# Optimization experiments

Hardware: AMD Instinct MI355X
Metric: run time of the kernel (lower is better)

Reference implementation:

```python
import jax, jax.numpy as jnp
import numpy as np

H = 16          # nhead
EPS = 1e-5      # LayerNorm eps (torch default)


def _layernorm(x, g, b):
    mu = jnp.mean(x, axis=-1, keepdims=True)
    var = jnp.mean(jnp.square(x - mu), axis=-1, keepdims=True)
    return (x - mu) * jax.lax.rsqrt(var + EPS) * g + b


def setup_inputs() -> dict:
    key = jax.random.key(0)
    ks = jax.random.split(key, 8)
    B, L, D, F = 256, 64, 1024, 4096
    s = 0.02
    return {
        "src": jax.random.normal(ks[0], (B, L, D), jnp.float32),
        "Wq": jax.random.normal(ks[1], (D, D), jnp.float32) * s,
        "bq": jnp.zeros((D,), jnp.float32),
        "Wk": jax.random.normal(ks[2], (D, D), jnp.float32) * s,
        "bk": jnp.zeros((D,), jnp.float32),
        "Wv": jax.random.normal(ks[3], (D, D), jnp.float32) * s,
        "bv": jnp.zeros((D,), jnp.float32),
        "Wo": jax.random.normal(ks[4], (D, D), jnp.float32) * s,
        "bo": jnp.zeros((D,), jnp.float32),
        "rel_bias": jax.random.normal(ks[5], (H, 2 * L - 1), jnp.float32) * s,
        "W1": jax.random.normal(ks[6], (D, F), jnp.float32) * s,
        "b1": jnp.zeros((F,), jnp.float32),
        "W2": jax.random.normal(ks[7], (F, D), jnp.float32) * s,
        "b2": jnp.zeros((D,), jnp.float32),
        "g1": jnp.ones((D,), jnp.float32),
        "be1": jnp.zeros((D,), jnp.float32),
        "g2": jnp.ones((D,), jnp.float32),
        "be2": jnp.zeros((D,), jnp.float32),
    }


def reference(src, Wq, bq, Wk, bk, Wv, bv, Wo, bo, rel_bias,
              W1, b1, W2, b2, g1, be1, g2, be2):
    B, L, D = src.shape
    dh = D // H
    # --- relative multi-head attention ---
    q = (src @ Wq + bq).reshape(B, L, H, dh)
    k = (src @ Wk + bk).reshape(B, L, H, dh)
    v = (src @ Wv + bv).reshape(B, L, H, dh)
    scores = jnp.einsum('bqhd,bkhd->bhqk', q, k) / jnp.sqrt(jnp.float32(dh))
    # relative position bias lookup: index i - j + (L-1) into (H, 2L-1) table
    rel_idx = jnp.arange(L)[:, None] - jnp.arange(L)[None, :] + (L - 1)  # (L,L)
    scores = scores + rel_bias[:, rel_idx]  # broadcast (H,L,L) over batch
    attn = jax.nn.softmax(scores, axis=-1)
    ctx = jnp.einsum('bhqk,bkhd->bqhd', attn, v).reshape(B, L, D)
    attn_out = ctx @ Wo + bo
    # --- residual + LN + FFN + residual + LN (dropout = eval no-op) ---
    x = _layernorm(src + attn_out, g1, be1)
    ff = jax.nn.gelu(x @ W1 + b1) @ W2 + b2
    return _layernorm(x + ff, g2, be2)
```

## Files before the change

### kernel.cpp

```cpp
#include <hip/hip_runtime.h>

typedef __bf16 bf16;
typedef __attribute__((ext_vector_type(8))) __bf16 bf16x8;
typedef __attribute__((ext_vector_type(4))) __bf16 bf16x4;
typedef __attribute__((ext_vector_type(4))) float f32x4;

#define N_TOK 16384
#define DMODEL 1024
#define FDIM 4096
#define NHEAD 16

__device__ __forceinline__ void gload_lds16(const bf16* g, bf16* l) {
  __builtin_amdgcn_global_load_lds(
      (const __attribute__((address_space(1))) void*)g,
      (__attribute__((address_space(3))) void*)l,
      16, 0, 0);
}

__device__ __forceinline__ float gelu_fast(float x) {
  float z2 = 1.5957691216057308f * (x + 0.044715f * x * x * x);
  return x / (1.0f + __expf(-z2));
}

__global__ __launch_bounds__(256) void cvt_copy(const float* __restrict__ x,
                                                bf16* __restrict__ y) {
  size_t i = ((size_t)blockIdx.x * 256 + threadIdx.x) * 8;
  float4 a = *(const float4*)(x + i);
  float4 b = *(const float4*)(x + i + 4);
  bf16x8 o;
  o[0] = (bf16)a.x; o[1] = (bf16)a.y; o[2] = (bf16)a.z; o[3] = (bf16)a.w;
  o[4] = (bf16)b.x; o[5] = (bf16)b.y; o[6] = (bf16)b.z; o[7] = (bf16)b.w;
  *(bf16x8*)(y + i) = o;
}

__global__ void convt(const float* __restrict__ src, bf16* __restrict__ dst,
                      int R, int C) {
  __shared__ float tile[32][33];
  int c0 = blockIdx.x * 32, r0 = blockIdx.y * 32;
  int tx = threadIdx.x, ty = threadIdx.y;
#pragma unroll
  for (int i = 0; i < 4; ++i)
    tile[ty * 4 + i][tx] = src[(size_t)(r0 + ty * 4 + i) * C + c0 + tx];
  __syncthreads();
#pragma unroll
  for (int i = 0; i < 4; ++i)
    dst[(size_t)(c0 + ty * 4 + i) * R + r0 + tx] = (bf16)tile[tx][ty * 4 + i];
}

template <int BM_, int RES, int GELU, int SPLIT3>
__global__ __launch_bounds__(512) void gemm_c(
    const bf16* __restrict__ A, const bf16* __restrict__ BT,
    const float* __restrict__ bias, const float* __restrict__ bias2,
    const float* __restrict__ bias3, const float* __restrict__ resf,
    const bf16* __restrict__ resb, bf16* __restrict__ C,
    bf16* __restrict__ C2, bf16* __restrict__ C3,
    int M, int N, int K) {
  constexpr int ALOADS = BM_ / 64;
  constexpr int MH = BM_ / 32;
  constexpr int MQ = MH / 2;
  __shared__ alignas(16) bf16 sA[2][BM_ * 64];
  __shared__ alignas(16) bf16 sB[2][256 * 64];

  const int tid = threadIdx.x;
  const int lane = tid & 63, wv = tid >> 6;
  const int wr = wv >> 2, wc = wv & 3;
  const int r16 = lane & 15, hk = lane >> 4;

  const int nbn = N >> 8;
  const int cpx = gridDim.x >> 3;
  const int swz = ((int)blockIdx.x & 7) * cpx + ((int)blockIdx.x >> 3);
  const int row0 = (swz / nbn) * BM_, col0 = (swz % nbn) << 8;

  const bf16* Ab = A + (size_t)row0 * K;
  const bf16* Bb = BT + (size_t)col0 * K;

  const bf16* gA[ALOADS];
  const bf16* gB[4];
#pragma unroll
  for (int l = 0; l < ALOADS; ++l) {
    int g = l * 512 + tid, r = g >> 3, p = g & 7;
    gA[l] = Ab + (size_t)r * K + ((p ^ (r & 7)) << 3);
  }
#pragma unroll
  for (int l = 0; l < 4; ++l) {
    int g = l * 512 + tid, r = g >> 3, p = g & 7;
    gB[l] = Bb + (size_t)r * K + ((p ^ (r & 7)) << 3);
  }

  auto stageA = [&](int buf, int kt) {
    const size_t ko = (size_t)kt << 6;
#pragma unroll
    for (int l = 0; l < ALOADS; ++l)
      gload_lds16(gA[l] + ko, &sA[buf][(l * 512 + tid) * 8]);
  };
  auto stageB = [&](int buf, int kt) {
    const size_t ko = (size_t)kt << 6;
#pragma unroll
    for (int l = 0; l < 4; ++l)
      gload_lds16(gB[l] + ko, &sB[buf][(l * 512 + tid) * 8]);
  };
  auto frag = [&](const bf16* s, int row, int kc) -> bf16x8 {
    return *(const bf16x8*)(s + row * 64 + (kc ^ ((row & 7) * 8)));
  };

  f32x4 acc[MH][4] = {};
  bf16x8 aF[MQ][2], bF0[2][2], bF1[2][2];

  const int nt = K >> 6;
  stageA(0, 0); stageB(0, 0);
  stageA(1, 1); stageB(1, 1);
  if constexpr (BM_ == 256) asm volatile("s_waitcnt vmcnt(8)" ::: "memory");
  else                      asm volatile("s_waitcnt vmcnt(6)" ::: "memory");
  __builtin_amdgcn_s_barrier();

  for (int kt = 0; kt < nt; ++kt) {
    const int cb = kt & 1;
    const bf16* sa = &sA[cb][0];
    const bf16* sb = &sB[cb][0];
    const bool pf = (kt + 2 < nt);

#pragma unroll
    for (int m = 0; m < MQ; ++m)
#pragma unroll
      for (int ks = 0; ks < 2; ++ks)
        aF[m][ks] = frag(sa, wr * (BM_ / 2) + m * 16 + r16, ks * 32 + hk * 8);
#pragma unroll
    for (int n = 0; n < 2; ++n)
#pragma unroll
      for (int ks = 0; ks < 2; ++ks)
        bF0[n][ks] = frag(sb, wc * 64 + n * 16 + r16, ks * 32 + hk * 8);
    __builtin_amdgcn_s_barrier();
    __builtin_amdgcn_s_setprio(1);
#pragma unroll
    for (int ks = 0; ks < 2; ++ks)
#pragma unroll
      for (int m = 0; m < MQ; ++m)
#pragma unroll
        for (int n = 0; n < 2; ++n)
          acc[m][n] = __builtin_amdgcn_mfma_f32_16x16x32_bf16(bF0[n][ks], aF[m][ks], acc[m][n], 0, 0, 0);
    __builtin_amdgcn_s_setprio(0);
    __builtin_amdgcn_s_barrier();

#pragma unroll
    for (int n = 0; n < 2; ++n)
#pragma unroll
      for (int ks = 0; ks < 2; ++ks)
        bF1[n][ks] = frag(sb, wc * 64 + (2 + n) * 16 + r16, ks * 32 + hk * 8);
    __builtin_amdgcn_s_barrier();
    __builtin_amdgcn_s_setprio(1);
#pragma unroll
    for (int ks = 0; ks < 2; ++ks)
#pragma unroll
      for (int m = 0; m < MQ; ++m)
#pragma unroll
        for (int n = 0; n < 2; ++n)
          acc[m][2 + n] = __builtin_amdgcn_mfma_f32_16x16x32_bf16(bF1[n][ks], aF[m][ks], acc[m][2 + n], 0, 0, 0);
    __builtin_amdgcn_s_setprio(0);
    __builtin_amdgcn_s_barrier();

#pragma unroll
    for (int m = 0; m < MQ; ++m)
#pragma unroll
      for (int ks = 0; ks < 2; ++ks)
        aF[m][ks] = frag(sa, wr * (BM_ / 2) + (MQ + m) * 16 + r16, ks * 32 + hk * 8);
    if (pf) stageB(cb, kt + 2);
    __builtin_amdgcn_s_barrier();
    __builtin_amdgcn_s_setprio(1);
#pragma unroll
    for (int ks = 0; ks < 2; ++ks)
#pragma unroll
      for (int m = 0; m < MQ; ++m)
#pragma unroll
        for (int n = 0; n < 2; ++n)
          acc[MQ + m][2 + n] = __builtin_amdgcn_mfma_f32_16x16x32_bf16(bF1[n][ks], aF[m][ks], acc[MQ + m][2 + n], 0, 0, 0);
    __builtin_amdgcn_s_setprio(0);
    __builtin_amdgcn_s_barrier();

    if (pf) stageA(cb, kt + 2);
    __builtin_amdgcn_s_setprio(1);
#pragma unroll
    for (int ks = 0; ks < 2; ++ks)
#pragma unroll
      for (int m = 0; m < MQ; ++m)
#pragma unroll
        for (int n = 0; n < 2; ++n)
          acc[MQ + m][n] = __builtin_amdgcn_mfma_f32_16x16x32_bf16(bF0[n][ks], aF[m][ks], acc[MQ + m][n], 0, 0, 0);
    __builtin_amdgcn_s_setprio(0);
    if (pf) {
      if constexpr (BM_ == 256) asm volatile("s_waitcnt vmcnt(8)" ::: "memory");
      else                      asm volatile("s_waitcnt vmcnt(6)" ::: "memory");
    } else if (kt + 1 < nt) {
      asm volatile("s_waitcnt vmcnt(0)" ::: "memory");
    }
    __builtin_amdgcn_s_barrier();
  }

  bf16* Cp = C;
  const float* bp = bias;
  int ldc = N, colb = col0;
  if constexpr (SPLIT3) {
    int grp = col0 >> 10;
    Cp = grp == 0 ? C : (grp == 1 ? C2 : C3);
    bp = grp == 0 ? bias : (grp == 1 ? bias2 : bias3);
    ldc = 1024;
    colb = col0 & 1023;
  }
#pragma unroll
  for (int m = 0; m < MH; ++m) {
    int row = row0 + wr * (BM_ / 2) + m * 16 + r16;
#pragma unroll
    for (int n = 0; n < 4; ++n) {
      int col = colb + wc * 64 + n * 16 + hk * 4;
      f32x4 b4 = *(const f32x4*)&bp[col];
      f32x4 v;
#pragma unroll
      for (int r = 0; r < 4; ++r) v[r] = acc[m][n][r] + b4[r];
      if (RES == 1) {
        f32x4 rr = *(const f32x4*)&resf[(size_t)row * ldc + col];
#pragma unroll
        for (int r = 0; r < 4; ++r) v[r] += rr[r];
      }
      if (RES == 2) {
        bf16x4 rb = *(const bf16x4*)&resb[(size_t)row * ldc + col];
#pragma unroll
        for (int r = 0; r < 4; ++r) v[r] += (float)rb[r];
      }
      bf16x4 o;
#pragma unroll
      for (int r = 0; r < 4; ++r) {
        float x = v[r];
        if (GELU) x = gelu_fast(x);
        o[r] = (bf16)x;
      }
      *(bf16x4*)&Cp[(size_t)row * ldc + col] = o;
    }
  }
}

__global__ __launch_bounds__(256) void attn_k(
    const bf16* q, const bf16* __restrict__ k,
    const bf16* __restrict__ v, const float* __restrict__ rel,
    bf16* ctx) {
  __shared__ alignas(16) bf16 lQ[64 * 64];
  __shared__ alignas(16) bf16 lK[64 * 64];
  __shared__ alignas(16) bf16 lVt[64 * 64];
  __shared__ alignas(16) bf16 lP[4][16 * 64];
  __shared__ float lrel[128];

  const int bh = blockIdx.x;
  const int b = bh >> 4, h = bh & 15;
  const int tid = threadIdx.x;
  const size_t base = (size_t)(b * 64) * DMODEL + h * 64;

#pragma unroll
  for (int i = 0; i < 2; ++i) {
    int j = (tid >> 3) + i * 32;
    int d0 = (tid & 7) * 8;
    *(bf16x8*)&lQ[j * 64 + d0] = *(const bf16x8*)(q + base + (size_t)j * DMODEL + d0);
    *(bf16x8*)&lK[j * 64 + d0] = *(const bf16x8*)(k + base + (size_t)j * DMODEL + d0);
    bf16x8 vvv = *(const bf16x8*)(v + base + (size_t)j * DMODEL + d0);
#pragma unroll
    for (int u = 0; u < 8; ++u) lVt[(d0 + u) * 64 + j] = vvv[u];
  }
  if (tid < 127) lrel[tid] = rel[h * 127 + tid];
  __syncthreads();

  const int lane = tid & 63, w = tid >> 6;
  const int r16 = lane & 15, hk = lane >> 4;

  f32x4 s[4] = {};
#pragma unroll
  for (int dstep = 0; dstep < 2; ++dstep) {
    bf16x8 aq = *(const bf16x8*)&lQ[(w * 16 + r16) * 64 + dstep * 32 + hk * 8];
#pragma unroll
    for (int n = 0; n < 4; ++n) {
      bf16x8 bk_ = *(const bf16x8*)&lK[(n * 16 + r16) * 64 + dstep * 32 + hk * 8];
      s[n] = __builtin_amdgcn_mfma_f32_16x16x32_bf16(aq, bk_, s[n], 0, 0, 0);
    }
  }

  float p[16];
#pragma unroll
  for (int n = 0; n < 4; ++n)
#pragma unroll
    for (int r = 0; r < 4; ++r) {
      int i = w * 16 + hk * 4 + r;
      int j = n * 16 + r16;
      p[n * 4 + r] = s[n][r] * 0.125f + lrel[i - j + 63];
    }
#pragma unroll
  for (int r = 0; r < 4; ++r) {
    float m = fmaxf(fmaxf(p[r], p[4 + r]), fmaxf(p[8 + r], p[12 + r]));
#pragma unroll
    for (int off = 1; off < 16; off <<= 1) m = fmaxf(m, __shfl_xor(m, off));
    float sum = 0.f;
#pragma unroll
    for (int n = 0; n < 4; ++n) {
      p[n * 4 + r] = __expf(p[n * 4 + r] - m);
      sum += p[n * 4 + r];
    }
#pragma unroll
    for (int off = 1; off < 16; off <<= 1) sum += __shfl_xor(sum, off);
    float inv = 1.0f / sum;
#pragma unroll
    for (int n = 0; n < 4; ++n) p[n * 4 + r] *= inv;
  }
#pragma unroll
  for (int n = 0; n < 4; ++n)
#pragma unroll
    for (int r = 0; r < 4; ++r)
      lP[w][(hk * 4 + r) * 64 + n * 16 + r16] = (bf16)p[n * 4 + r];
  __syncthreads();

  f32x4 o[4] = {};
#pragma unroll
  for (int ks = 0; ks < 2; ++ks) {
    bf16x8 ap = *(const bf16x8*)&lP[w][r16 * 64 + ks * 32 + hk * 8];
#pragma unroll
    for (int n = 0; n < 4; ++n) {
      bf16x8 bv_ = *(const bf16x8*)&lVt[(n * 16 + r16) * 64 + ks * 32 + hk * 8];
      o[n] = __builtin_amdgcn_mfma_f32_16x16x32_bf16(ap, bv_, o[n], 0, 0, 0);
    }
  }
#pragma unroll
  for (int n = 0; n < 4; ++n)
#pragma unroll
    for (int r = 0; r < 4; ++r) {
      int trow = b * 64 + w * 16 + hk * 4 + r;
      ctx[(size_t)trow * DMODEL + h * 64 + n * 16 + r16] = (bf16)o[n][r];
    }
}

template <int F32OUT>
__global__ __launch_bounds__(256) void layernorm_k(
    const bf16* __restrict__ x, const float* __restrict__ g,
    const float* __restrict__ be, bf16* __restrict__ ob,
    float* __restrict__ of) {
  int row = blockIdx.x * 4 + (threadIdx.x >> 6);
  int lane = threadIdx.x & 63;
  const bf16* xr = x + (size_t)row * DMODEL + lane * 16;
  bf16x8 v0 = *(const bf16x8*)xr;
  bf16x8 v1 = *(const bf16x8*)(xr + 8);
  float f[16];
#pragma unroll
  for (int j = 0; j < 8; ++j) { f[j] = (float)v0[j]; f[8 + j] = (float)v1[j]; }
  float s = 0.f, sq = 0.f;
#pragma unroll
  for (int j = 0; j < 16; ++j) { s += f[j]; sq += f[j] * f[j]; }
#pragma unroll
  for (int off = 1; off < 64; off <<= 1) {
    s += __shfl_xor(s, off);
    sq += __shfl_xor(sq, off);
  }
  float mean = s * (1.0f / DMODEL);
  float var = sq * (1.0f / DMODEL) - mean * mean;
  float rstd = rsqrtf(var + 1e-5f);
  const float* gp = g + lane * 16;
  const float* bp = be + lane * 16;
  if (F32OUT) {
    float* op = of + (size_t)row * DMODEL + lane * 16;
#pragma unroll
    for (int j = 0; j < 16; ++j)
      op[j] = (f[j] - mean) * rstd * gp[j] + bp[j];
  } else {
    bf16x8 o0, o1;
#pragma unroll
    for (int j = 0; j < 8; ++j) {
      o0[j] = (bf16)((f[j] - mean) * rstd * gp[j] + bp[j]);
      o1[j] = (bf16)((f[8 + j] - mean) * rstd * gp[8 + j] + bp[8 + j]);
    }
    bf16* op = ob + (size_t)row * DMODEL + lane * 16;
    *(bf16x8*)op = o0;
    *(bf16x8*)(op + 8) = o1;
  }
}

extern "C" void kernel_launch(void* const* d_in, const int* in_sizes, int n_in,
                              void* d_out, int out_size, void* d_ws, size_t ws_size,
                              hipStream_t stream) {
  (void)in_sizes; (void)n_in; (void)out_size;
  const float* src = (const float*)d_in[0];
  const float* Wq  = (const float*)d_in[1];
  const float* bq  = (const float*)d_in[2];
  const float* Wk  = (const float*)d_in[3];
  const float* bk  = (const float*)d_in[4];
  const float* Wv  = (const float*)d_in[5];
  const float* bv  = (const float*)d_in[6];
  const float* Wo  = (const float*)d_in[7];
  const float* bo  = (const float*)d_in[8];
  const float* rel = (const float*)d_in[9];
  const float* W1  = (const float*)d_in[10];
  const float* b1  = (const float*)d_in[11];
  const float* W2  = (const float*)d_in[12];
  const float* b2  = (const float*)d_in[13];
  const float* g1  = (const float*)d_in[14];
  const float* be1 = (const float*)d_in[15];
  const float* g2  = (const float*)d_in[16];
  const float* be2 = (const float*)d_in[17];

  char* ws = (char*)d_ws;
  const size_t MiB = 1ull << 20;
  bf16* srcb = (bf16*)(ws + 0 * MiB);
  bf16* qb   = (bf16*)(ws + 32 * MiB);
  bf16* WqT  = (bf16*)(ws + 64 * MiB);
  bf16* WkT  = (bf16*)(ws + 66 * MiB);
  bf16* WvT  = (bf16*)(ws + 68 * MiB);
  bf16* WoT  = (bf16*)(ws + 70 * MiB);
  bf16* W1T  = (bf16*)(ws + 72 * MiB);
  bf16* W2T  = (bf16*)(ws + 80 * MiB);
  bf16* hbuf = (bf16*)(ws + 0 * MiB);
  float* lnout = (float*)(ws + 0 * MiB);
  bf16* kb = (bf16*)d_out;
  bf16* vb = (bf16*)((char*)d_out + 32 * MiB);
  bf16* y1 = kb;
  bf16* xb = vb;
  const bool bigws = (ws_size >= 121 * MiB);
  bf16* y2 = bigws ? (bf16*)(ws + 88 * MiB) : kb;

  cvt_copy<<<(N_TOK * DMODEL) / 2048, 256, 0, stream>>>(src, srcb);
  dim3 tb(32, 8);
  convt<<<dim3(32, 32), tb, 0, stream>>>(Wq, WqT, 1024, 1024);
  convt<<<dim3(32, 32), tb, 0, stream>>>(Wk, WkT, 1024, 1024);
  convt<<<dim3(32, 32), tb, 0, stream>>>(Wv, WvT, 1024, 1024);
  convt<<<dim3(32, 32), tb, 0, stream>>>(Wo, WoT, 1024, 1024);
  convt<<<dim3(128, 32), tb, 0, stream>>>(W1, W1T, 1024, 4096);
  convt<<<dim3(32, 128), tb, 0, stream>>>(W2, W2T, 4096, 1024);

  const int gQKV3 = (N_TOK / 256) * (3072 / 256);
  gemm_c<256, 0, 0, 1><<<gQKV3, 512, 0, stream>>>(
      srcb, WqT, bq, bk, bv, nullptr, nullptr, qb, kb, vb, N_TOK, 3072, DMODEL);

  attn_k<<<256 * NHEAD, 256, 0, stream>>>(qb, kb, vb, rel, qb);

  const int gD = (N_TOK / 256) * (DMODEL / 256);
  gemm_c<256, 1, 0, 0><<<gD, 512, 0, stream>>>(
      qb, WoT, bo, nullptr, nullptr, src, nullptr, y1, nullptr, nullptr, N_TOK, DMODEL, DMODEL);
  layernorm_k<0><<<N_TOK / 4, 256, 0, stream>>>(y1, g1, be1, xb, nullptr);

  const int CH = 8192;
  const int gF1 = (CH / 256) * (FDIM / 256);
  const int gF2 = (CH / 128) * (DMODEL / 256);
  for (int c = 0; c < 2; ++c) {
    const bf16* xc = xb + (size_t)c * CH * DMODEL;
    bf16* yc = y2 + (size_t)c * CH * DMODEL;
    gemm_c<256, 0, 1, 0><<<gF1, 512, 0, stream>>>(
        xc, W1T, b1, nullptr, nullptr, nullptr, nullptr, hbuf, nullptr, nullptr, CH, FDIM, DMODEL);
    gemm_c<128, 2, 0, 0><<<gF2, 512, 0, stream>>>(
        hbuf, W2T, b2, nullptr, nullptr, nullptr, xc, yc, nullptr, nullptr, CH, DMODEL, FDIM);
  }
  if (bigws) {
    layernorm_k<1><<<N_TOK / 4, 256, 0, stream>>>(y2, g2, be2, nullptr, (float*)d_out);
  } else {
    layernorm_k<1><<<N_TOK / 4, 256, 0, stream>>>(y2, g2, be2, nullptr, lnout);
    hipMemcpyAsync(d_out, lnout, (size_t)N_TOK * DMODEL * 4, hipMemcpyDeviceToDevice, stream);
  }
}
```

Measured before the change: 613.3 us.

## Software-pipeline LDS fragment reads across k-tiles in GEMM main loop

Restructures the GEMM k-loop so the low-half A and B fragments for the next k-tile are read from the other LDS buffer while the current tile's last MFMA phases run. The loop is unrolled by two with ping-pong fragment registers, and the global prefetch order is changed to B before A. This aims to hide LDS read latency behind MFMA work. It adds register pressure, a vmcnt(0) wait in every tile, and assumes an even number of k-tiles.

```diff
diff --git a/kernel.cpp b/kernel.cpp
--- a/kernel.cpp
+++ b/kernel.cpp
@@ -56,8 +56,8 @@
     bf16* __restrict__ C2, bf16* __restrict__ C3,
     int M, int N, int K) {
   constexpr int ALOADS = BM_ / 64;
-  constexpr int MH = BM_ / 32;
-  constexpr int MQ = MH / 2;
+  constexpr int MQ = BM_ / 64;
+  constexpr int MH = 2 * MQ;
   __shared__ alignas(16) bf16 sA[2][BM_ * 64];
   __shared__ alignas(16) bf16 sB[2][256 * 64];
 
@@ -104,96 +104,97 @@
   };
 
   f32x4 acc[MH][4] = {};
-  bf16x8 aF[MQ][2], bF0[2][2], bF1[2][2];
+  bf16x8 aL[MQ][2], aH[MQ][2], bH[2][2], bLa[2][2], bLb[2][2];
 
   const int nt = K >> 6;
-  stageA(0, 0); stageB(0, 0);
-  stageA(1, 1); stageB(1, 1);
+  stageB(0, 0); stageA(0, 0);
+  stageB(1, 1); stageA(1, 1);
   if constexpr (BM_ == 256) asm volatile("s_waitcnt vmcnt(8)" ::: "memory");
   else                      asm volatile("s_waitcnt vmcnt(6)" ::: "memory");
   __builtin_amdgcn_s_barrier();
-
-  for (int kt = 0; kt < nt; ++kt) {
-    const int cb = kt & 1;
-    const bf16* sa = &sA[cb][0];
-    const bf16* sb = &sB[cb][0];
-    const bool pf = (kt + 2 < nt);
-
-#pragma unroll
-    for (int m = 0; m < MQ; ++m)
-#pragma unroll
-      for (int ks = 0; ks < 2; ++ks)
-        aF[m][ks] = frag(sa, wr * (BM_ / 2) + m * 16 + r16, ks * 32 + hk * 8);
-#pragma unroll
-    for (int n = 0; n < 2; ++n)
-#pragma unroll
-      for (int ks = 0; ks < 2; ++ks)
-        bF0[n][ks] = frag(sb, wc * 64 + n * 16 + r16, ks * 32 + hk * 8);
-    __builtin_amdgcn_s_barrier();
-    __builtin_amdgcn_s_setprio(1);
+#pragma unroll
+  for (int m = 0; m < MQ; ++m)
 #pragma unroll
     for (int ks = 0; ks < 2; ++ks)
-#pragma unroll
-      for (int m = 0; m < MQ; ++m)
-#pragma unroll
-        for (int n = 0; n < 2; ++n)
-          acc[m][n] = __builtin_amdgcn_mfma_f32_16x16x32_bf16(bF0[n][ks], aF[m][ks], acc[m][n], 0, 0, 0);
-    __builtin_amdgcn_s_setprio(0);
-    __builtin_amdgcn_s_barrier();
-
-#pragma unroll
-    for (int n = 0; n < 2; ++n)
-#pragma unroll
-      for (int ks = 0; ks < 2; ++ks)
-        bF1[n][ks] = frag(sb, wc * 64 + (2 + n) * 16 + r16, ks * 32 + hk * 8);
-    __builtin_amdgcn_s_barrier();
-    __builtin_amdgcn_s_setprio(1);
+      aL[m][ks] = frag(&sA[0][0], wr * (BM_ / 2) + m * 16 + r16, ks * 32 + hk * 8);
+#pragma unroll
+  for (int n = 0; n < 2; ++n)
 #pragma unroll
     for (int ks = 0; ks < 2; ++ks)
-#pragma unroll
-      for (int m = 0; m < MQ; ++m)
-#pragma unroll
-        for (int n = 0; n < 2; ++n)
-          acc[m][2 + n] = __builtin_amdgcn_mfma_f32_16x16x32_bf16(bF1[n][ks], aF[m][ks], acc[m][2 + n], 0, 0, 0);
-    __builtin_amdgcn_s_setprio(0);
-    __builtin_amdgcn_s_barrier();
-
-#pragma unroll
-    for (int m = 0; m < MQ; ++m)
-#pragma unroll
-      for (int ks = 0; ks < 2; ++ks)
-        aF[m][ks] = frag(sa, wr * (BM_ / 2) + (MQ + m) * 16 + r16, ks * 32 + hk * 8);
-    if (pf) stageB(cb, kt + 2);
-    __builtin_amdgcn_s_barrier();
-    __builtin_amdgcn_s_setprio(1);
-#pragma unroll
-    for (int ks = 0; ks < 2; ++ks)
-#pragma unroll
-      for (int m = 0; m < MQ; ++m)
-#pragma unroll
-        for (int n = 0; n < 2; ++n)
-          acc[MQ + m][2 + n] = __builtin_amdgcn_mfma_f32_16x16x32_bf16(bF1[n][ks], aF[m][ks], acc[MQ + m][2 + n], 0, 0, 0);
-    __builtin_amdgcn_s_setprio(0);
-    __builtin_amdgcn_s_barrier();
-
-    if (pf) stageA(cb, kt + 2);
-    __builtin_amdgcn_s_setprio(1);
-#pragma unroll
-    for (int ks = 0; ks < 2; ++ks)
-#pragma unroll
-      for (int m = 0; m < MQ; ++m)
-#pragma unroll
-        for (int n = 0; n < 2; ++n)
-          acc[MQ + m][n] = __builtin_amdgcn_mfma_f32_16x16x32_bf16(bF0[n][ks], aF[m][ks], acc[MQ + m][n], 0, 0, 0);
-    __builtin_amdgcn_s_setprio(0);
-    if (pf) {
-      if constexpr (BM_ == 256) asm volatile("s_waitcnt vmcnt(8)" ::: "memory");
-      else                      asm volatile("s_waitcnt vmcnt(6)" ::: "memory");
-    } else if (kt + 1 < nt) {
-      asm volatile("s_waitcnt vmcnt(0)" ::: "memory");
-    }
-    __builtin_amdgcn_s_barrier();
-  }
+      bLa[n][ks] = frag(&sB[0][0], wc * 64 + n * 16 + r16, ks * 32 + hk * 8);
+
+#define TILE_BODY(t, sa, sb, saN, sbN, bLcur, bLnxt)                           \
+  {                                                                            \
+    const bool rd1 = ((t) + 1 < nt), st2 = ((t) + 2 < nt);                     \
+                                       \
+    _Pragma("unroll") for (int n = 0; n < 2; ++n)                              \
+      _Pragma("unroll") for (int ks = 0; ks < 2; ++ks)                         \
+        bH[n][ks] = frag(sb, wc * 64 + (2 + n) * 16 + r16, ks * 32 + hk * 8);  \
+    __builtin_amdgcn_s_barrier();                                              \
+    __builtin_amdgcn_s_setprio(1);                                             \
+    _Pragma("unroll") for (int ks = 0; ks < 2; ++ks)                           \
+      _Pragma("unroll") for (int m = 0; m < MQ; ++m)                           \
+        _Pragma("unroll") for (int n = 0; n < 2; ++n)                          \
+          acc[m][n] = __builtin_amdgcn_mfma_f32_16x16x32_bf16(                 \
+              bLcur[n][ks], aL[m][ks], acc[m][n], 0, 0, 0);                    \
+    __builtin_amdgcn_s_setprio(0);                                             \
+    __builtin_amdgcn_s_barrier();                                              \
+          \
+    _Pragma("unroll") for (int m = 0; m < MQ; ++m)                             \
+      _Pragma("unroll") for (int ks = 0; ks < 2; ++ks)                         \
+        aH[m][ks] = frag(sa, wr * (BM_ / 2) + (MQ + m) * 16 + r16,             \
+                         ks * 32 + hk * 8);                                    \
+    __builtin_amdgcn_s_barrier();                                              \
+    __builtin_amdgcn_s_setprio(1);                                             \
+    _Pragma("unroll") for (int ks = 0; ks < 2; ++ks)                           \
+      _Pragma("unroll") for (int m = 0; m < MQ; ++m)                           \
+        _Pragma("unroll") for (int n = 0; n < 2; ++n)                          \
+          acc[m][2 + n] = __builtin_amdgcn_mfma_f32_16x16x32_bf16(             \
+              bH[n][ks], aL[m][ks], acc[m][2 + n], 0, 0, 0);                   \
+    __builtin_amdgcn_s_setprio(0);                                             \
+    asm volatile("s_waitcnt vmcnt(0)" ::: "memory");                           \
+    __builtin_amdgcn_s_barrier();                                              \
+                         \
+    if (rd1) {                                                                 \
+      _Pragma("unroll") for (int m = 0; m < MQ; ++m)                           \
+        _Pragma("unroll") for (int ks = 0; ks < 2; ++ks)                       \
+          aL[m][ks] = frag(saN, wr * (BM_ / 2) + m * 16 + r16,                 \
+                           ks * 32 + hk * 8);                                  \
+    }                                                                          \
+    if (st2) stageB((t) & 1, (t) + 2);                                         \
+    __builtin_amdgcn_s_barrier();                                              \
+    __builtin_amdgcn_s_setprio(1);                                             \
+    _Pragma("unroll") for (int ks = 0; ks < 2; ++ks)                           \
+      _Pragma("unroll") for (int m = 0; m < MQ; ++m)                           \
+        _Pragma("unroll") for (int n = 0; n < 2; ++n)                          \
+          acc[MQ + m][2 + n] = __builtin_amdgcn_mfma_f32_16x16x32_bf16(        \
+              bH[n][ks], aH[m][ks], acc[MQ + m][2 + n], 0, 0, 0);              \
+    __builtin_amdgcn_s_setprio(0);                                             \
+    __builtin_amdgcn_s_barrier();                                              \
+               \
+    if (rd1) {                                                                 \
+      _Pragma("unroll") for (int n = 0; n < 2; ++n)                            \
+        _Pragma("unroll") for (int ks = 0; ks < 2; ++ks)                       \
+          bLnxt[n][ks] = frag(sbN, wc * 64 + n * 16 + r16, ks * 32 + hk * 8);  \
+    }                                                                          \
+    if (st2) stageA((t) & 1, (t) + 2);                                         \
+    __builtin_amdgcn_s_barrier();                                              \
+    __builtin_amdgcn_s_setprio(1);                                             \
+    _Pragma("unroll") for (int ks = 0; ks < 2; ++ks)                           \
+      _Pragma("unroll") for (int m = 0; m < MQ; ++m)                           \
+        _Pragma("unroll") for (int n = 0; n < 2; ++n)                          \
+          acc[MQ + m][n] = __builtin_amdgcn_mfma_f32_16x16x32_bf16(            \
+              bLcur[n][ks], aH[m][ks], acc[MQ + m][n], 0, 0, 0);               \
+    __builtin_amdgcn_s_setprio(0);                                             \
+    __builtin_amdgcn_s_barrier();                                              \
+  }
+
+  for (int it = 0; it < nt / 2; ++it) {
+    const int e = 2 * it;
+    TILE_BODY(e,     &sA[0][0], &sB[0][0], &sA[1][0], &sB[1][0], bLa, bLb);
+    TILE_BODY(e + 1, &sA[1][0], &sB[1][0], &sA[0][0], &sB[0][0], bLb, bLa);
+  }
+#undef TILE_BODY
 
   bf16* Cp = C;
   const float* bp = bias;
```

After: 978.6 us. 1.6x slower.

## Add dedicated triple-buffered FFN2 GEMM kernel with split-phase MFMA scheduling

Applied to the files above, without the earlier changes.

Replaces the generic gemm_c call for the second FFN projection (K=4096, N=1024) with a specialized 128x256-tile kernel. It uses three LDS buffers with a two-stage-ahead prefetch, splits each k-step into two MFMA halves with barriers and priority hints, and issues the next stage's loads between them to overlap global-to-LDS traffic with compute. It also applies an XCD-aware block swizzle. This adds a large LDS footprint (about 144 KB) and hard-coded tile assumptions.

```diff
diff --git a/kernel.cpp b/kernel.cpp
--- a/kernel.cpp
+++ b/kernel.cpp
@@ -233,6 +233,132 @@
         o[r] = (bf16)x;
       }
       *(bf16x4*)&Cp[(size_t)row * ldc + col] = o;
+    }
+  }
+}
+
+__global__ __launch_bounds__(512) void gemm_d(
+    const bf16* __restrict__ A, const bf16* __restrict__ BT,
+    const float* __restrict__ bias, const bf16* __restrict__ resb,
+    bf16* __restrict__ C, int M, int N, int K) {
+  __shared__ alignas(16) bf16 sA[3][128 * 64];
+  __shared__ alignas(16) bf16 sB[3][256 * 64];
+
+  const int tid = threadIdx.x;
+  const int lane = tid & 63, wv = tid >> 6;
+  const int wr = wv >> 2, wc = wv & 3;
+  const int r16 = lane & 15, hk = lane >> 4;
+
+  const int nbn = N >> 8;
+  const int cpx = gridDim.x >> 3;
+  const int swz = ((int)blockIdx.x & 7) * cpx + ((int)blockIdx.x >> 3);
+  const int row0 = (swz / nbn) * 128, col0 = (swz % nbn) << 8;
+
+  const bf16* Ab = A + (size_t)row0 * K;
+  const bf16* Bb = BT + (size_t)col0 * K;
+
+  const bf16* gA[2];
+  const bf16* gB[4];
+#pragma unroll
+  for (int l = 0; l < 2; ++l) {
+    int g = l * 512 + tid, r = g >> 3, p = g & 7;
+    gA[l] = Ab + (size_t)r * K + ((p ^ (r & 7)) << 3);
+  }
+#pragma unroll
+  for (int l = 0; l < 4; ++l) {
+    int g = l * 512 + tid, r = g >> 3, p = g & 7;
+    gB[l] = Bb + (size_t)r * K + ((p ^ (r & 7)) << 3);
+  }
+
+  auto stage = [&](int buf, int kt) {
+    const size_t ko = (size_t)kt << 6;
+#pragma unroll
+    for (int l = 0; l < 2; ++l)
+      gload_lds16(gA[l] + ko, &sA[buf][(l * 512 + tid) * 8]);
+#pragma unroll
+    for (int l = 0; l < 4; ++l)
+      gload_lds16(gB[l] + ko, &sB[buf][(l * 512 + tid) * 8]);
+  };
+  auto frag = [&](const bf16* s, int row, int kc) -> bf16x8 {
+    return *(const bf16x8*)(s + row * 64 + (kc ^ ((row & 7) * 8)));
+  };
+
+  f32x4 acc[4][4] = {};
+  bf16x8 aF[4][2], bF0[2][2], bF1[2][2];
+
+  const int nt = K >> 6;
+  stage(0, 0);
+  stage(1, 1);
+  asm volatile("s_waitcnt vmcnt(6)" ::: "memory");
+  __builtin_amdgcn_s_barrier();
+
+  int cur = 0;
+  for (int kt = 0; kt < nt; ++kt) {
+    const bf16* sa = &sA[cur][0];
+    const bf16* sb = &sB[cur][0];
+    const int nx2 = (cur + 2 >= 3) ? cur - 1 : cur + 2;
+    const bool pf = (kt + 2 < nt);
+
+#pragma unroll
+    for (int m = 0; m < 4; ++m)
+#pragma unroll
+      for (int ks = 0; ks < 2; ++ks)
+        aF[m][ks] = frag(sa, wr * 64 + m * 16 + r16, ks * 32 + hk * 8);
+#pragma unroll
+    for (int n = 0; n < 2; ++n)
+#pragma unroll
+      for (int ks = 0; ks < 2; ++ks)
+        bF0[n][ks] = frag(sb, wc * 64 + n * 16 + r16, ks * 32 + hk * 8);
+    __builtin_amdgcn_s_barrier();
+    __builtin_amdgcn_s_setprio(1);
+#pragma unroll
+    for (int ks = 0; ks < 2; ++ks)
+#pragma unroll
+      for (int m = 0; m < 4; ++m)
+#pragma unroll
+        for (int n = 0; n < 2; ++n)
+          acc[m][n] = __builtin_amdgcn_mfma_f32_16x16x32_bf16(bF0[n][ks], aF[m][ks], acc[m][n], 0, 0, 0);
+    __builtin_amdgcn_s_setprio(0);
+    __builtin_amdgcn_s_barrier();
+
+#pragma unroll
+    for (int n = 0; n < 2; ++n)
+#pragma unroll
+      for (int ks = 0; ks < 2; ++ks)
+        bF1[n][ks] = frag(sb, wc * 64 + (2 + n) * 16 + r16, ks * 32 + hk * 8);
+    if (pf) stage(nx2, kt + 2);
+    __builtin_amdgcn_s_barrier();
+    __builtin_amdgcn_s_setprio(1);
+#pragma unroll
+    for (int ks = 0; ks < 2; ++ks)
+#pragma unroll
+      for (int m = 0; m < 4; ++m)
+#pragma unroll
+        for (int n = 0; n < 2; ++n)
+          acc[m][2 + n] = __builtin_amdgcn_mfma_f32_16x16x32_bf16(bF1[n][ks], aF[m][ks], acc[m][2 + n], 0, 0, 0);
+    __builtin_amdgcn_s_setprio(0);
+    if (pf) {
+      asm volatile("s_waitcnt vmcnt(6)" ::: "memory");
+    } else if (kt + 1 < nt) {
+      asm volatile("s_waitcnt vmcnt(0)" ::: "memory");
+    }
+    __builtin_amdgcn_s_barrier();
+    cur = (cur + 1 == 3) ? 0 : cur + 1;
+  }
+
+#pragma unroll
+  for (int m = 0; m < 4; ++m) {
+    int row = row0 + wr * 64 + m * 16 + r16;
+#pragma unroll
+    for (int n = 0; n < 4; ++n) {
+      int col = col0 + wc * 64 + n * 16 + hk * 4;
+      f32x4 b4 = *(const f32x4*)&bias[col];
+      bf16x4 rb = *(const bf16x4*)&resb[(size_t)row * N + col];
+      bf16x4 o;
+#pragma unroll
+      for (int r = 0; r < 4; ++r)
+        o[r] = (bf16)(acc[m][n][r] + b4[r] + (float)rb[r]);
+      *(bf16x4*)&C[(size_t)row * N + col] = o;
     }
   }
 }
@@ -445,8 +571,7 @@
     bf16* yc = y2 + (size_t)c * CH * DMODEL;
     gemm_c<256, 0, 1, 0><<<gF1, 512, 0, stream>>>(
         xc, W1T, b1, nullptr, nullptr, nullptr, nullptr, hbuf, nullptr, nullptr, CH, FDIM, DMODEL);
-    gemm_c<128, 2, 0, 0><<<gF2, 512, 0, stream>>>(
-        hbuf, W2T, b2, nullptr, nullptr, nullptr, xc, yc, nullptr, nullptr, CH, DMODEL, FDIM);
+    gemm_d<<<gF2, 512, 0, stream>>>(hbuf, W2T, b2, xc, yc, CH, DMODEL, FDIM);
   }
   if (bigws) {
     layernorm_k<1><<<N_TOK / 4, 256, 0, stream>>>(y2, g2, be2, nullptr, (float*)d_out);
```

Result: no change. 607.0 us (-1.0%).

## Use 128x256 GEMM tiles everywhere with a triple-buffered LDS pipeline

Applied to the files above, without the earlier changes.

Replaces the templated BM GEMM with a fixed 128-row tile kernel that keeps three LDS stages instead of two. Each k-step issues one combined A+B prefetch two stages ahead, and the loop body drops from four barrier-separated MFMA phases to two. All GEMMs (QKV, Wo, FFN1, FFN2) now use 128x256 tiles, which doubles the grid for the former 256-row launches. The trade is less A/B reuse per block and more LDS use per block (144 KB), which may lower occupancy, in exchange for fewer barriers and deeper prefetch.

```diff
diff --git a/kernel.cpp b/kernel.cpp
--- a/kernel.cpp
+++ b/kernel.cpp
@@ -47,19 +47,16 @@
     dst[(size_t)(c0 + ty * 4 + i) * R + r0 + tx] = (bf16)tile[tx][ty * 4 + i];
 }
 
-template <int BM_, int RES, int GELU, int SPLIT3>
-__global__ __launch_bounds__(512) void gemm_c(
+template <int RES, int GELU, int SPLIT3>
+__global__ __launch_bounds__(512) void gemm_e(
     const bf16* __restrict__ A, const bf16* __restrict__ BT,
     const float* __restrict__ bias, const float* __restrict__ bias2,
     const float* __restrict__ bias3, const float* __restrict__ resf,
     const bf16* __restrict__ resb, bf16* __restrict__ C,
     bf16* __restrict__ C2, bf16* __restrict__ C3,
     int M, int N, int K) {
-  constexpr int ALOADS = BM_ / 64;
-  constexpr int MH = BM_ / 32;
-  constexpr int MQ = MH / 2;
-  __shared__ alignas(16) bf16 sA[2][BM_ * 64];
-  __shared__ alignas(16) bf16 sB[2][256 * 64];
+  __shared__ alignas(16) bf16 sA[3][128 * 64];
+  __shared__ alignas(16) bf16 sB[3][256 * 64];
 
   const int tid = threadIdx.x;
   const int lane = tid & 63, wv = tid >> 6;
@@ -69,15 +66,15 @@
   const int nbn = N >> 8;
   const int cpx = gridDim.x >> 3;
   const int swz = ((int)blockIdx.x & 7) * cpx + ((int)blockIdx.x >> 3);
-  const int row0 = (swz / nbn) * BM_, col0 = (swz % nbn) << 8;
+  const int row0 = (swz / nbn) * 128, col0 = (swz % nbn) << 8;
 
   const bf16* Ab = A + (size_t)row0 * K;
   const bf16* Bb = BT + (size_t)col0 * K;
 
-  const bf16* gA[ALOADS];
+  const bf16* gA[2];
   const bf16* gB[4];
 #pragma unroll
-  for (int l = 0; l < ALOADS; ++l) {
+  for (int l = 0; l < 2; ++l) {
     int g = l * 512 + tid, r = g >> 3, p = g & 7;
     gA[l] = Ab + (size_t)r * K + ((p ^ (r & 7)) << 3);
   }
@@ -87,14 +84,11 @@
     gB[l] = Bb + (size_t)r * K + ((p ^ (r & 7)) << 3);
   }
 
-  auto stageA = [&](int buf, int kt) {
+  auto stage = [&](int buf, int kt) {
     const size_t ko = (size_t)kt << 6;
 #pragma unroll
-    for (int l = 0; l < ALOADS; ++l)
+    for (int l = 0; l < 2; ++l)
       gload_lds16(gA[l] + ko, &sA[buf][(l * 512 + tid) * 8]);
-  };
-  auto stageB = [&](int buf, int kt) {
-    const size_t ko = (size_t)kt << 6;
 #pragma unroll
     for (int l = 0; l < 4; ++l)
       gload_lds16(gB[l] + ko, &sB[buf][(l * 512 + tid) * 8]);
@@ -103,27 +97,27 @@
     return *(const bf16x8*)(s + row * 64 + (kc ^ ((row & 7) * 8)));
   };
 
-  f32x4 acc[MH][4] = {};
-  bf16x8 aF[MQ][2], bF0[2][2], bF1[2][2];
+  f32x4 acc[4][4] = {};
+  bf16x8 aF[4][2], bF0[2][2], bF1[2][2];
 
   const int nt = K >> 6;
-  stageA(0, 0); stageB(0, 0);
-  stageA(1, 1); stageB(1, 1);
-  if constexpr (BM_ == 256) asm volatile("s_waitcnt vmcnt(8)" ::: "memory");
-  else                      asm volatile("s_waitcnt vmcnt(6)" ::: "memory");
+  stage(0, 0);
+  stage(1, 1);
+  asm volatile("s_waitcnt vmcnt(6)" ::: "memory");
   __builtin_amdgcn_s_barrier();
 
+  int cur = 0;
   for (int kt = 0; kt < nt; ++kt) {
-    const int cb = kt & 1;
-    const bf16* sa = &sA[cb][0];
-    const bf16* sb = &sB[cb][0];
+    const bf16* sa = &sA[cur][0];
+    const bf16* sb = &sB[cur][0];
+    const int nx2 = (cur + 2 >= 3) ? cur - 1 : cur + 2;
     const bool pf = (kt + 2 < nt);
 
 #pragma unroll
-    for (int m = 0; m < MQ; ++m)
+    for (int m = 0; m < 4; ++m)
 #pragma unroll
       for (int ks = 0; ks < 2; ++ks)
-        aF[m][ks] = frag(sa, wr * (BM_ / 2) + m * 16 + r16, ks * 32 + hk * 8);
+        aF[m][ks] = frag(sa, wr * 64 + m * 16 + r16, ks * 32 + hk * 8);
 #pragma unroll
     for (int n = 0; n < 2; ++n)
 #pragma unroll
@@ -134,7 +128,7 @@
 #pragma unroll
     for (int ks = 0; ks < 2; ++ks)
 #pragma unroll
-      for (int m = 0; m < MQ; ++m)
+      for (int m = 0; m < 4; ++m)
 #pragma unroll
         for (int n = 0; n < 2; ++n)
           acc[m][n] = __builtin_amdgcn_mfma_f32_16x16x32_bf16(bF0[n][ks], aF[m][ks], acc[m][n], 0, 0, 0);
@@ -146,53 +140,24 @@
 #pragma unroll
       for (int ks = 0; ks < 2; ++ks)
         bF1[n][ks] = frag(sb, wc * 64 + (2 + n) * 16 + r16, ks * 32 + hk * 8);
+    if (pf) stage(nx2, kt + 2);
     __builtin_amdgcn_s_barrier();
     __builtin_amdgcn_s_setprio(1);
 #pragma unroll
     for (int ks = 0; ks < 2; ++ks)
 #pragma unroll
-      for (int m = 0; m < MQ; ++m)
+      for (int m = 0; m < 4; ++m)
 #pragma unroll
         for (int n = 0; n < 2; ++n)
           acc[m][2 + n] = __builtin_amdgcn_mfma_f32_16x16x32_bf16(bF1[n][ks], aF[m][ks], acc[m][2 + n], 0, 0, 0);
     __builtin_amdgcn_s_setprio(0);
-    __builtin_amdgcn_s_barrier();
-
-#pragma unroll
-    for (int m = 0; m < MQ; ++m)
-#pragma unroll
-      for (int ks = 0; ks < 2; ++ks)
-        aF[m][ks] = frag(sa, wr * (BM_ / 2) + (MQ + m) * 16 + r16, ks * 32 + hk * 8);
-    if (pf) stageB(cb, kt + 2);
-    __builtin_amdgcn_s_barrier();
-    __builtin_amdgcn_s_setprio(1);
-#pragma unroll
-    for (int ks = 0; ks < 2; ++ks)
-#pragma unroll
-      for (int m = 0; m < MQ; ++m)
-#pragma unroll
-        for (int n = 0; n < 2; ++n)
-          acc[MQ + m][2 + n] = __builtin_amdgcn_mfma_f32_16x16x32_bf16(bF1[n][ks], aF[m][ks], acc[MQ + m][2 + n], 0, 0, 0);
-    __builtin_amdgcn_s_setprio(0);
-    __builtin_amdgcn_s_barrier();
-
-    if (pf) stageA(cb, kt + 2);
-    __builtin_amdgcn_s_setprio(1);
-#pragma unroll
-    for (int ks = 0; ks < 2; ++ks)
-#pragma unroll
-      for (int m = 0; m < MQ; ++m)
-#pragma unroll
-        for (int n = 0; n < 2; ++n)
-          acc[MQ + m][n] = __builtin_amdgcn_mfma_f32_16x16x32_bf16(bF0[n][ks], aF[m][ks], acc[MQ + m][n], 0, 0, 0);
-    __builtin_amdgcn_s_setprio(0);
     if (pf) {
-      if constexpr (BM_ == 256) asm volatile("s_waitcnt vmcnt(8)" ::: "memory");
-      else                      asm volatile("s_waitcnt vmcnt(6)" ::: "memory");
+      asm volatile("s_waitcnt vmcnt(6)" ::: "memory");
     } else if (kt + 1 < nt) {
       asm volatile("s_waitcnt vmcnt(0)" ::: "memory");
     }
     __builtin_amdgcn_s_barrier();
+    cur = (cur + 1 == 3) ? 0 : cur + 1;
   }
 
   bf16* Cp = C;
@@ -206,8 +171,8 @@
     colb = col0 & 1023;
   }
 #pragma unroll
-  for (int m = 0; m < MH; ++m) {
-    int row = row0 + wr * (BM_ / 2) + m * 16 + r16;
+  for (int m = 0; m < 4; ++m) {
+    int row = row0 + wr * 64 + m * 16 + r16;
 #pragma unroll
     for (int n = 0; n < 4; ++n) {
       int col = colb + wc * 64 + n * 16 + hk * 4;
@@ -426,26 +391,26 @@
   convt<<<dim3(128, 32), tb, 0, stream>>>(W1, W1T, 1024, 4096);
   convt<<<dim3(32, 128), tb, 0, stream>>>(W2, W2T, 4096, 1024);
 
-  const int gQKV3 = (N_TOK / 256) * (3072 / 256);
-  gemm_c<256, 0, 0, 1><<<gQKV3, 512, 0, stream>>>(
+  const int gQKV3 = (N_TOK / 128) * (3072 / 256);
+  gemm_e<0, 0, 1><<<gQKV3, 512, 0, stream>>>(
       srcb, WqT, bq, bk, bv, nullptr, nullptr, qb, kb, vb, N_TOK, 3072, DMODEL);
 
   attn_k<<<256 * NHEAD, 256, 0, stream>>>(qb, kb, vb, rel, qb);
 
-  const int gD = (N_TOK / 256) * (DMODEL / 256);
-  gemm_c<256, 1, 0, 0><<<gD, 512, 0, stream>>>(
+  const int gD = (N_TOK / 128) * (DMODEL / 256);
+  gemm_e<1, 0, 0><<<gD, 512, 0, stream>>>(
       qb, WoT, bo, nullptr, nullptr, src, nullptr, y1, nullptr, nullptr, N_TOK, DMODEL, DMODEL);
   layernorm_k<0><<<N_TOK / 4, 256, 0, stream>>>(y1, g1, be1, xb, nullptr);
 
   const int CH = 8192;
-  const int gF1 = (CH / 256) * (FDIM / 256);
+  const int gF1 = (CH / 128) * (FDIM / 256);
   const int gF2 = (CH / 128) * (DMODEL / 256);
   for (int c = 0; c < 2; ++c) {
     const bf16* xc = xb + (size_t)c * CH * DMODEL;
     bf16* yc = y2 + (size_t)c * CH * DMODEL;
-    gemm_c<256, 0, 1, 0><<<gF1, 512, 0, stream>>>(
+    gemm_e<0, 1, 0><<<gF1, 512, 0, stream>>>(
         xc, W1T, b1, nullptr, nullptr, nullptr, nullptr, hbuf, nullptr, nullptr, CH, FDIM, DMODEL);
-    gemm_c<128, 2, 0, 0><<<gF2, 512, 0, stream>>>(
+    gemm_e<2, 0, 0><<<gF2, 512, 0, stream>>>(
         hbuf, W2T, b2, nullptr, nullptr, nullptr, xc, yc, nullptr, nullptr, CH, DMODEL, FDIM);
   }
   if (bigws) {
```

New measurement: 679.0 us. 1.11x slower.
